# Kernel tuning notes

Measured on AMD Instinct MI355X. Metric: run time of the kernel, lower is better.

The kernel has to match this reference:

```python
import jax, jax.numpy as jnp
import numpy as np

EPS = 1e-5  # BatchNorm1d default eps


def gcn_conv(x, src, dst, w, b, n):
    # src/dst already include self-loops. Symmetric normalization D^-1/2 (A+I) D^-1/2.
    deg = jnp.zeros((n,), x.dtype).at[dst].add(1.0)
    dinv = jnp.where(deg > 0, jax.lax.rsqrt(jnp.maximum(deg, 1.0)), 0.0)
    norm = dinv[src] * dinv[dst]                      # [E+N]
    h = x @ w                                          # [B, N, H]
    msg = h[:, src, :] * norm[None, :, None]           # gather + scale  [B, E+N, H]
    agg = jnp.zeros_like(h).at[:, dst, :].add(msg)     # scatter-add
    return agg + b


def batch_norm(h, gamma, beta):
    # training-mode BN over the flattened (B*N) axis, biased variance (torch BN forward)
    mu = h.mean(axis=(0, 1))
    var = ((h - mu) ** 2).mean(axis=(0, 1))
    return (h - mu) * jax.lax.rsqrt(var + EPS) * gamma + beta


def reference(x, edge_index, W1, b1, W2, b2, gamma1, beta1, gamma2, beta2, Wc, bc):
    n = x.shape[1]
    loops = jnp.arange(n)
    src = jnp.concatenate([edge_index[0], loops])
    dst = jnp.concatenate([edge_index[1], loops])
    h = jax.nn.relu(gcn_conv(x, src, dst, W1, b1, n))
    h = batch_norm(h, gamma1, beta1)
    # dropout(p=0.2) treated as identity (eval / deterministic reference)
    h = jax.nn.relu(gcn_conv(h, src, dst, W2, b2, n))
    h = batch_norm(h, gamma2, beta2)
    out = (h @ Wc + bc).squeeze(-1)                    # [B, N]
    return out


def setup_inputs() -> dict:
    key = jax.random.key(0)
    ks = jax.random.split(key, 8)
    B, N, E, F, H = 4, 20000, 320000, 64, 128
    s = lambda fan: 1.0 / np.sqrt(fan)
    return {
        "x": jax.random.normal(ks[0], (B, N, F), dtype=jnp.float32),
        "edge_index": jax.random.randint(ks[1], (2, E), 0, N, dtype=jnp.int64),
        "W1": jax.random.normal(ks[2], (F, H), dtype=jnp.float32) * s(F),
        "b1": jnp.zeros((H,), jnp.float32),
        "W2": jax.random.normal(ks[3], (H, H), dtype=jnp.float32) * s(H),
        "b2": jnp.zeros((H,), jnp.float32),
        "gamma1": jnp.ones((H,), jnp.float32),
        "beta1": jnp.zeros((H,), jnp.float32),
        "gamma2": jnp.ones((H,), jnp.float32),
        "beta2": jnp.zeros((H,), jnp.float32),
        "Wc": jax.random.normal(ks[4], (H, 1), dtype=jnp.float32) * s(H),
        "bc": jnp.zeros((1,), jnp.float32),
    }
```

## Files before the change

### kernel.cpp

```cpp
#include <hip/hip_runtime.h>

constexpr int Bb = 4;
constexpr int Nn = 20000;
constexpr int Ff = 64;
constexpr int Hh = 128;
constexpr float BN_EPS = 1e-5f;
constexpr int NSLOTS = 64;
constexpr int NB = (Nn + 1023) / 1024;

typedef __attribute__((ext_vector_type(8))) short bf16x8;
typedef __attribute__((ext_vector_type(4))) float f32x4;

__device__ inline unsigned f2bf(float f) {
    unsigned u = __float_as_uint(f);
    return (u + 0x7fffu + ((u >> 16) & 1u)) >> 16;
}
__device__ inline unsigned pack2(float lo, float hi) { return f2bf(lo) | (f2bf(hi) << 16); }
__device__ inline float bf_lo(unsigned w) { return __uint_as_float(w << 16); }
__device__ inline float bf_hi(unsigned w) { return __uint_as_float(w & 0xffff0000u); }

template <int NU>
__device__ inline void ldrow(unsigned* u, const unsigned* p) {
    if constexpr (NU == 2) { const uint2 t = *(const uint2*)p; u[0] = t.x; u[1] = t.y; }
    else { const uint4 t = *(const uint4*)p; u[0] = t.x; u[1] = t.y; u[2] = t.z; u[3] = t.w; }
}
template <int NU>
__device__ inline void acc_row(float* a, const unsigned* u, float nm) {
#pragma unroll
    for (int c = 0; c < NU; ++c) {
        a[2 * c]     = fmaf(nm, bf_lo(u[c]), a[2 * c]);
        a[2 * c + 1] = fmaf(nm, bf_hi(u[c]), a[2 * c + 1]);
    }
}

__global__ __launch_bounds__(256) void k_pre(const int* __restrict__ dst, int E,
                                             int NDEG,
                                             int* __restrict__ deg,
                                             const float* __restrict__ x,
                                             unsigned* __restrict__ xb,
                                             const float* __restrict__ W1,
                                             unsigned short* __restrict__ WTf) {
    const int b = blockIdx.x;
    if (b < NDEG) {
        const int e = b * 256 + threadIdx.x;
        if (e < E) atomicAdd(&deg[dst[e]], 1);
    } else if (b < NDEG + (Bb * Nn * 32) / 256) {
        const int o = (b - NDEG) * 256 + threadIdx.x;
        const int n   = o >> 7;
        const int rem = o & 127;
        const int bb  = rem >> 5;
        const int c2  = rem & 31;
        const float2 v = *(const float2*)&x[(((size_t)bb * Nn + n) * 64) + c2 * 2];
        xb[o] = pack2(v.x, v.y);
    } else {
        const int f = (b - NDEG - (Bb * Nn * 32) / 256) * 256 + threadIdx.x;
        if (f < 128 * Ff) {
            const int j = f & 7, lane = (f >> 3) & 63, rest = f >> 9;
            const int ks = rest & 1, tt = rest >> 1;
            const int col = tt * 16 + (lane & 15);
            const int k = ks * 32 + ((lane >> 4) << 3) + j;
            WTf[f] = (unsigned short)f2bf(W1[(size_t)k * 128 + col]);
        }
    }
}

__global__ __launch_bounds__(1024) void k_scanall(const int* __restrict__ deg,
                                                  int* __restrict__ rowptr,
                                                  int* __restrict__ cursor,
                                                  float* __restrict__ dinv) {
    __shared__ int red[16];
    __shared__ int woff[16];
    __shared__ int base_s;
    const int tid = threadIdx.x, lane = tid & 63, wid = tid >> 6;
    const int b = blockIdx.x;

    int pre = 0;
    for (int i = tid; i < b * 1024; i += 1024) pre += deg[i] + 1;
#pragma unroll
    for (int d = 32; d; d >>= 1) pre += __shfl_down(pre, d);
    if (lane == 0) red[wid] = pre;
    __syncthreads();
    if (tid == 0) {
        int s = 0;
        for (int w = 0; w < 16; ++w) s += red[w];
        base_s = s;
    }

    const int i = b * 1024 + tid;
    const int cnt = (i < Nn) ? deg[i] + 1 : 0;
    int v = cnt;
#pragma unroll
    for (int d = 1; d < 64; d <<= 1) {
        const int t = __shfl_up(v, d);
        if (lane >= d) v += t;
    }
    __syncthreads();
    if (lane == 63) red[wid] = v;
    __syncthreads();
    if (wid == 0) {
        const int orig = (lane < 16) ? red[lane] : 0;
        int w = orig;
#pragma unroll
        for (int d = 1; d < 16; d <<= 1) {
            const int t = __shfl_up(w, d);
            if (lane >= d) w += t;
        }
        if (lane < 16) woff[lane] = w - orig;
    }
    __syncthreads();
    if (i < Nn) {
        const int excl = base_s + woff[wid] + (v - cnt);
        rowptr[i] = excl;
        cursor[i] = excl;
        dinv[i] = rsqrtf((float)cnt);
        if (i == Nn - 1) rowptr[Nn] = excl + cnt;
    }
}

__global__ void k_fill(const int* __restrict__ src, const int* __restrict__ dst, int E,
                       const float* __restrict__ dinv, int* __restrict__ cursor,
                       int* __restrict__ csr_src, float* __restrict__ csr_norm,
                       float* __restrict__ nsum) {
    int t = blockIdx.x * blockDim.x + threadIdx.x;
    int s, d;
    if (t < E) { s = src[t]; d = dst[t]; }
    else if (t < E + Nn) { s = d = t - E; }
    else return;
    int pos = atomicAdd(&cursor[d], 1);
    const float nm = dinv[s] * dinv[d];
    csr_src[pos]  = s;
    csr_norm[pos] = nm;
    atomicAdd(&nsum[d], nm);
}

__global__ __launch_bounds__(128) void k_prep2(const float* __restrict__ gsum,
                                               const float* __restrict__ gsq,
                                               const float* __restrict__ gamma,
                                               const float* __restrict__ beta,
                                               const float* __restrict__ W2,
                                               unsigned short* __restrict__ WT2f,
                                               float* __restrict__ shW2) {
    __shared__ float sc_s[128], sh_s[128];
    const int c = threadIdx.x;
    float s = 0.f, q = 0.f;
    for (int j = 0; j < NSLOTS; ++j) { s += gsum[j * 128 + c]; q += gsq[j * 128 + c]; }
    const float inv = 1.0f / (float)(Bb * Nn);
    const float mu  = s * inv;
    const float var = q * inv - mu * mu;
    const float sc  = gamma[c] * rsqrtf(var + BN_EPS);
    sc_s[c] = sc;
    sh_s[c] = beta[c] - mu * sc;
    __syncthreads();
    if (blockIdx.x < 64) {
#pragma unroll
        for (int i = 0; i < 2; ++i) {
            const int f = blockIdx.x * 256 + i * 128 + c;
            const int j = f & 7, lane = (f >> 3) & 63, rest = f >> 9;
            const int ks = rest & 3, tt = rest >> 2;
            const int col = tt * 16 + (lane & 15);
            const int k = ks * 32 + ((lane >> 4) << 3) + j;
            WT2f[f] = (unsigned short)f2bf(sc_s[k] * W2[(size_t)k * 128 + col]);
        }
    } else {
        float a = 0.f;
        for (int k = 0; k < 128; ++k) a = fmaf(sh_s[k], W2[(size_t)k * 128 + c], a);
        shW2[c] = a;
    }
}

template <int K, bool L2E>
__global__ __launch_bounds__(64, 6) void k_fmm(const unsigned* __restrict__ G,
                                               const int* __restrict__ rowptr,
                                               const int* __restrict__ csr_src,
                                               const float* __restrict__ csr_norm,
                                               const unsigned short* __restrict__ WTf,
                                               const float* __restrict__ bias,
                                               const float* __restrict__ nsum,
                                               const float* __restrict__ shW2,
                                               unsigned short* __restrict__ Yout,
                                               float* __restrict__ gsum,
                                               float* __restrict__ gsq) {
    constexpr int NKS = K / 32;
    constexpr int AST = K + 8;
    constexpr int NU = K / 32;
    constexpr int ROWU = Bb * K / 2;
    __shared__ alignas(16) unsigned short sA[16 * AST];

    const int lane = threadIdx.x;
    const int cg = lane & 15, kg = lane >> 4;
    const int g = blockIdx.x;
    const int row0 = g * 16;

#pragma unroll
    for (int j = 0; j < 4; ++j) {
        const int v = g * 4 + j;
        const int beg = rowptr[v], end = rowptr[v + 1];
        float a[2 * NU];
#pragma unroll
        for (int c = 0; c < 2 * NU; ++c) a[c] = 0.f;
        int e = beg;
        for (; e + 8 <= end; e += 8) {
            unsigned u[8][NU];
            int si[8];
#pragma unroll
            for (int q = 0; q < 8; ++q) si[q] = csr_src[e + q];
#pragma unroll
            for (int q = 0; q < 8; ++q)
                ldrow<NU>(u[q], G + (size_t)si[q] * ROWU + lane * NU);
#pragma unroll
            for (int q = 0; q < 8; ++q) acc_row<NU>(a, u[q], csr_norm[e + q]);
        }
        for (; e + 4 <= end; e += 4) {
            unsigned u[4][NU];
            int si[4];
#pragma unroll
            for (int q = 0; q < 4; ++q) si[q] = csr_src[e + q];
#pragma unroll
            for (int q = 0; q < 4; ++q)
                ldrow<NU>(u[q], G + (size_t)si[q] * ROWU + lane * NU);
#pragma unroll
            for (int q = 0; q < 4; ++q) acc_row<NU>(a, u[q], csr_norm[e + q]);
        }
        for (; e < end; ++e) {
            unsigned u[NU];
            ldrow<NU>(u, G + (size_t)csr_src[e] * ROWU + lane * NU);
            acc_row<NU>(a, u, csr_norm[e]);
        }
        const int row = j * 4 + kg;
        unsigned p[NU];
#pragma unroll
        for (int c = 0; c < NU; ++c) p[c] = pack2(a[2 * c], a[2 * c + 1]);
        if constexpr (NU == 2) *(uint2*)&sA[row * AST + cg * 4] = *(const uint2*)p;
        else                   *(uint4*)&sA[row * AST + cg * 8] = *(const uint4*)p;
    }

    f32x4 acc[8];
#pragma unroll
    for (int t = 0; t < 8; ++t) acc[t] = (f32x4){0.f, 0.f, 0.f, 0.f};
#pragma unroll
    for (int ks = 0; ks < NKS; ++ks) {
        const bf16x8 av = *(const bf16x8*)&sA[cg * AST + ks * 32 + kg * 8];
#pragma unroll
        for (int t = 0; t < 8; ++t) {
            const bf16x8 bv = *(const bf16x8*)&WTf[(size_t)((t * NKS + ks) * 64 + lane) * 8];
            acc[t] = __builtin_amdgcn_mfma_f32_16x16x32_bf16(av, bv, acc[t], 0, 0, 0);
        }
    }

    const int rbase = kg * 4;
    float ns = 0.f;
    if (L2E) ns = nsum[g * 4 + kg];
    float* gs = gsum + (size_t)(g & (NSLOTS - 1)) * 128;
    float* gq = gsq  + (size_t)(g & (NSLOTS - 1)) * 128;
#pragma unroll
    for (int t = 0; t < 8; ++t) {
        const int col = t * 16 + cg;
        float badd = bias[col];
        if (L2E) badd = fmaf(ns, shW2[col], badd);
        float s = 0.f, q = 0.f;
#pragma unroll
        for (int jj = 0; jj < 4; ++jj) {
            const float y = fmaxf(acc[t][jj] + badd, 0.f);
            Yout[(size_t)(row0 + rbase + jj) * 128 + col] = (unsigned short)f2bf(y);
            s += y; q = fmaf(y, y, q);
        }
        s += __shfl_xor(s, 16); s += __shfl_xor(s, 32);
        q += __shfl_xor(q, 16); q += __shfl_xor(q, 32);
        if (kg == 0) { atomicAdd(&gs[col], s); atomicAdd(&gq[col], q); }
    }
}

__global__ void k_bnfin2(const float* __restrict__ gsum, const float* __restrict__ gsq,
                         const float* __restrict__ gamma, const float* __restrict__ beta,
                         const float* __restrict__ Wc, const float* __restrict__ bc,
                         float* __restrict__ wcs, float* __restrict__ kc) {
    __shared__ float red[128];
    const int c = threadIdx.x;
    float s = 0.f, q = 0.f;
    for (int j = 0; j < NSLOTS; ++j) { s += gsum[j * 128 + c]; q += gsq[j * 128 + c]; }
    const float inv = 1.0f / (float)(Bb * Nn);
    const float mu  = s * inv;
    const float var = q * inv - mu * mu;
    const float sc  = gamma[c] * rsqrtf(var + BN_EPS);
    const float sh  = beta[c] - mu * sc;
    const float w   = Wc[c];
    wcs[c] = sc * w;
    red[c] = sh * w;
    __syncthreads();
    for (int st = 64; st; st >>= 1) {
        if (c < st) red[c] += red[c + st];
        __syncthreads();
    }
    if (c == 0) kc[0] = red[0] + bc[0];
}

__global__ __launch_bounds__(256) void k_cls(const unsigned* __restrict__ h2,
                                             const float* __restrict__ wcs,
                                             const float* __restrict__ kc,
                                             float* __restrict__ out) {
    __shared__ float sres[64];
    const int w = threadIdx.x >> 6;
    const int lane = threadIdx.x & 63;
    const int n0 = blockIdx.x * 16;
    const float2 wc = *(const float2*)&wcs[lane * 2];
#pragma unroll
    for (int jj = 0; jj < 4; ++jj) {
        const int node = n0 + w * 4 + jj;
#pragma unroll
        for (int b = 0; b < 4; ++b) {
            const size_t row = (size_t)node * 4 + b;
            const unsigned hv = h2[row * 64 + lane];
            float p = bf_lo(hv) * wc.x + bf_hi(hv) * wc.y;
#pragma unroll
            for (int off = 32; off; off >>= 1) p += __shfl_down(p, off);
            if (lane == 0) sres[b * 16 + w * 4 + jj] = p;
        }
    }
    __syncthreads();
    if (threadIdx.x < 64) {
        const int b = threadIdx.x >> 4, i = threadIdx.x & 15;
        out[(size_t)b * Nn + n0 + i] = sres[b * 16 + i] + kc[0];
    }
}

extern "C" void kernel_launch(void* const* d_in, const int* in_sizes, int n_in,
                              void* d_out, int out_size, void* d_ws, size_t ws_size,
                              hipStream_t stream) {
    const float* x      = (const float*)d_in[0];
    const int*   ei     = (const int*)d_in[1];
    const float* W1     = (const float*)d_in[2];
    const float* b1     = (const float*)d_in[3];
    const float* W2     = (const float*)d_in[4];
    const float* b2     = (const float*)d_in[5];
    const float* gamma1 = (const float*)d_in[6];
    const float* beta1  = (const float*)d_in[7];
    const float* gamma2 = (const float*)d_in[8];
    const float* beta2  = (const float*)d_in[9];
    const float* Wc     = (const float*)d_in[10];
    const float* bc     = (const float*)d_in[11];
    float* out = (float*)d_out;

    const int E = in_sizes[1] / 2;
    const int* src = ei;
    const int* dst = ei + E;

    char* ws = (char*)d_ws;
    size_t off = 0;
    auto alloc = [&](size_t bytes) -> char* {
        char* p = ws + off;
        off += (bytes + 255) & ~(size_t)255;
        return p;
    };
    int*      deg      = (int*)     alloc((size_t)Nn * 4);
    float*    nsum     = (float*)   alloc((size_t)Nn * 4);
    float*    gstat    = (float*)   alloc((size_t)4 * NSLOTS * 128 * 4);
    const size_t zspan = (size_t)((char*)(gstat + 4 * NSLOTS * 128) - (char*)deg);
    float* gsum1 = gstat;
    float* gsq1  = gstat + NSLOTS * 128;
    float* gsum2 = gstat + 2 * NSLOTS * 128;
    float* gsq2  = gstat + 3 * NSLOTS * 128;

    int*      cursor   = (int*)     alloc((size_t)Nn * 4);
    int*      rowptr   = (int*)     alloc((size_t)(Nn + 1) * 4);
    float*    dinv     = (float*)   alloc((size_t)Nn * 4);
    int*      csr_src  = (int*)     alloc((size_t)(E + Nn) * 4);
    float*    csr_norm = (float*)   alloc((size_t)(E + Nn) * 4);
    float*    wcs      = (float*)   alloc(128 * 4);
    float*    kc       = (float*)   alloc(256);
    unsigned short* WT1f = (unsigned short*)alloc((size_t)128 * Ff * 2);
    unsigned short* WT2f = (unsigned short*)alloc((size_t)128 * Hh * 2);
    float*          shW2 = (float*)         alloc((size_t)128 * 4);
    unsigned*       xb   = (unsigned*)      alloc((size_t)Nn * Bb * 32 * 4);
    unsigned short* h1b  = (unsigned short*)alloc((size_t)Bb * Nn * Hh * 2);
    unsigned short* h2b  = (unsigned short*)alloc((size_t)Bb * Nn * Hh * 2);

    (void)hipMemsetAsync(deg, 0, zspan, stream);

    const int NDEG = (E + 255) / 256;
    const int NCVT = (Bb * Nn * 32) / 256;
    k_pre<<<NDEG + NCVT + 32, 256, 0, stream>>>(dst, E, NDEG, deg, x, xb, W1, WT1f);
    k_scanall<<<NB, 1024, 0, stream>>>(deg, rowptr, cursor, dinv);
    k_fill<<<(E + Nn + 255) / 256, 256, 0, stream>>>(src, dst, E, dinv, cursor,
                                                     csr_src, csr_norm, nsum);

    k_fmm<Ff, false><<<Nn / 4, 64, 0, stream>>>(
        xb, rowptr, csr_src, csr_norm, WT1f, b1, nullptr, nullptr, h1b, gsum1, gsq1);
    k_prep2<<<65, 128, 0, stream>>>(gsum1, gsq1, gamma1, beta1, W2, WT2f, shW2);
    k_fmm<Hh, true><<<Nn / 4, 64, 0, stream>>>(
        (const unsigned*)h1b, rowptr, csr_src, csr_norm, WT2f, b2, nsum, shW2,
        h2b, gsum2, gsq2);
    k_bnfin2<<<1, Hh, 0, stream>>>(gsum2, gsq2, gamma2, beta2, Wc, bc, wcs, kc);

    k_cls<<<Nn / 16, 256, 0, stream>>>((const unsigned*)h2b, wcs, kc, out);
}
```

Baseline: 178.7 us.

## Halve nodes per wavefront in fused GCN kernel and stage output through LDS

Each 64-thread block now aggregates 2 nodes (8 batch-rows) instead of 4, which doubles the grid to expose more parallelism for the gather-bound aggregation. MFMA rows 8-15 are now wasted. The output tile is staged in shared memory and written with coalesced 16-byte stores instead of scattered 2-byte stores. The gather unroll depth for K=128 drops to 4, the launch-bounds occupancy hint goes from 6 to 8, and the BN partial-sum slots grow from 64 to 256 to reduce atomic contention. The cost is redundant MFMA work and twice as many blocks doing bias, stat and atomic epilogues.

```diff
diff --git a/kernel.cpp b/kernel.cpp
--- a/kernel.cpp
+++ b/kernel.cpp
@@ -5,7 +5,7 @@
 constexpr int Ff = 64;
 constexpr int Hh = 128;
 constexpr float BN_EPS = 1e-5f;
-constexpr int NSLOTS = 64;
+constexpr int NSLOTS = 256;
 constexpr int NB = (Nn + 1023) / 1024;
 
 typedef __attribute__((ext_vector_type(8))) short bf16x8;
@@ -169,7 +169,7 @@
 }
 
 template <int K, bool L2E>
-__global__ __launch_bounds__(64, 6) void k_fmm(const unsigned* __restrict__ G,
+__global__ __launch_bounds__(64, 8) void k_fmm(const unsigned* __restrict__ G,
                                                const int* __restrict__ rowptr,
                                                const int* __restrict__ csr_src,
                                                const float* __restrict__ csr_norm,
@@ -183,43 +183,34 @@
     constexpr int NKS = K / 32;
     constexpr int AST = K + 8;
     constexpr int NU = K / 32;
+    constexpr int UNR = (K == 128) ? 4 : 8;
     constexpr int ROWU = Bb * K / 2;
-    __shared__ alignas(16) unsigned short sA[16 * AST];
+    __shared__ alignas(16) unsigned short sA[16 * AST + (K == 64 ? 1024 : 0)];
+    unsigned short* const sO = (K == 64) ? &sA[16 * AST] : &sA[8 * AST];
 
     const int lane = threadIdx.x;
     const int cg = lane & 15, kg = lane >> 4;
     const int g = blockIdx.x;
-    const int row0 = g * 16;
-
-#pragma unroll
-    for (int j = 0; j < 4; ++j) {
-        const int v = g * 4 + j;
+    const int row0 = g * 8;
+
+#pragma unroll
+    for (int j = 0; j < 2; ++j) {
+        const int v = g * 2 + j;
         const int beg = rowptr[v], end = rowptr[v + 1];
         float a[2 * NU];
 #pragma unroll
         for (int c = 0; c < 2 * NU; ++c) a[c] = 0.f;
         int e = beg;
-        for (; e + 8 <= end; e += 8) {
-            unsigned u[8][NU];
-            int si[8];
-#pragma unroll
-            for (int q = 0; q < 8; ++q) si[q] = csr_src[e + q];
-#pragma unroll
-            for (int q = 0; q < 8; ++q)
+        for (; e + UNR <= end; e += UNR) {
+            unsigned u[UNR][NU];
+            int si[UNR];
+#pragma unroll
+            for (int q = 0; q < UNR; ++q) si[q] = csr_src[e + q];
+#pragma unroll
+            for (int q = 0; q < UNR; ++q)
                 ldrow<NU>(u[q], G + (size_t)si[q] * ROWU + lane * NU);
 #pragma unroll
-            for (int q = 0; q < 8; ++q) acc_row<NU>(a, u[q], csr_norm[e + q]);
-        }
-        for (; e + 4 <= end; e += 4) {
-            unsigned u[4][NU];
-            int si[4];
-#pragma unroll
-            for (int q = 0; q < 4; ++q) si[q] = csr_src[e + q];
-#pragma unroll
-            for (int q = 0; q < 4; ++q)
-                ldrow<NU>(u[q], G + (size_t)si[q] * ROWU + lane * NU);
-#pragma unroll
-            for (int q = 0; q < 4; ++q) acc_row<NU>(a, u[q], csr_norm[e + q]);
+            for (int q = 0; q < UNR; ++q) acc_row<NU>(a, u[q], csr_norm[e + q]);
         }
         for (; e < end; ++e) {
             unsigned u[NU];
@@ -249,24 +240,32 @@
 
     const int rbase = kg * 4;
     float ns = 0.f;
-    if (L2E) ns = nsum[g * 4 + kg];
+    if (L2E && kg < 2) ns = nsum[g * 2 + kg];
     float* gs = gsum + (size_t)(g & (NSLOTS - 1)) * 128;
     float* gq = gsq  + (size_t)(g & (NSLOTS - 1)) * 128;
 #pragma unroll
     for (int t = 0; t < 8; ++t) {
         const int col = t * 16 + cg;
-        float badd = bias[col];
-        if (L2E) badd = fmaf(ns, shW2[col], badd);
         float s = 0.f, q = 0.f;
-#pragma unroll
-        for (int jj = 0; jj < 4; ++jj) {
-            const float y = fmaxf(acc[t][jj] + badd, 0.f);
-            Yout[(size_t)(row0 + rbase + jj) * 128 + col] = (unsigned short)f2bf(y);
-            s += y; q = fmaf(y, y, q);
+        if (kg < 2) {
+            float badd = bias[col];
+            if (L2E) badd = fmaf(ns, shW2[col], badd);
+#pragma unroll
+            for (int jj = 0; jj < 4; ++jj) {
+                const float y = fmaxf(acc[t][jj] + badd, 0.f);
+                sO[(rbase + jj) * 128 + col] = (unsigned short)f2bf(y);
+                s += y; q = fmaf(y, y, q);
+            }
         }
         s += __shfl_xor(s, 16); s += __shfl_xor(s, 32);
         q += __shfl_xor(q, 16); q += __shfl_xor(q, 32);
         if (kg == 0) { atomicAdd(&gs[col], s); atomicAdd(&gq[col], q); }
+    }
+    const size_t obase = (size_t)row0 * 128;
+#pragma unroll
+    for (int h = 0; h < 2; ++h) {
+        const int i16 = h * 64 + lane;
+        *(uint4*)&Yout[obase + (size_t)i16 * 8] = *(const uint4*)&sO[i16 * 8];
     }
 }
 
@@ -383,10 +382,10 @@
     k_fill<<<(E + Nn + 255) / 256, 256, 0, stream>>>(src, dst, E, dinv, cursor,
                                                      csr_src, csr_norm, nsum);
 
-    k_fmm<Ff, false><<<Nn / 4, 64, 0, stream>>>(
+    k_fmm<Ff, false><<<Nn / 2, 64, 0, stream>>>(
         xb, rowptr, csr_src, csr_norm, WT1f, b1, nullptr, nullptr, h1b, gsum1, gsq1);
     k_prep2<<<65, 128, 0, stream>>>(gsum1, gsq1, gamma1, beta1, W2, WT2f, shW2);
-    k_fmm<Hh, true><<<Nn / 4, 64, 0, stream>>>(
+    k_fmm<Hh, true><<<Nn / 2, 64, 0, stream>>>(
         (const unsigned*)h1b, rowptr, csr_src, csr_norm, WT2f, b2, nsum, shW2,
         h2b, gsum2, gsq2);
     k_bnfin2<<<1, Hh, 0, stream>>>(gsum2, gsq2, gamma2, beta2, Wc, bc, wcs, kc);
```

New measurement: 201.0 us. 12.5% more time.
